# Kernel tuning notes

Hardware: AMD Instinct MI355X
Metric: run time of the kernel (lower is better)

## Reference

```python
import jax, jax.numpy as jnp
import numpy as np

N_EMBD = 768
N_HEAD = 12
HEAD_DIM = N_EMBD // N_HEAD


def setup_inputs() -> dict:
    key = jax.random.key(0)
    k1, k2, k3, k4, k5 = jax.random.split(key, 5)
    B, T, C = 8, 1024, N_EMBD
    s = 0.02
    return {
        "x": jax.random.normal(k1, (B, T, C), dtype=jnp.float32),
        "w_attn": jax.random.normal(k2, (C, 3 * C), dtype=jnp.float32) * s,
        "b_attn": jnp.zeros((3 * C,), dtype=jnp.float32),
        "w_proj": jax.random.normal(k3, (C, C), dtype=jnp.float32) * s,
        "b_proj": jnp.zeros((C,), dtype=jnp.float32),
    }


def reference(x, w_attn, b_attn, w_proj, b_proj):
    B, T, C = x.shape
    H, D = N_HEAD, HEAD_DIM
    qkv = x @ w_attn + b_attn                      # [B,T,3C]
    q, k, v = jnp.split(qkv, 3, axis=-1)
    # [B,H,T,D]
    q = q.reshape(B, T, H, D).transpose(0, 2, 1, 3)
    k = k.reshape(B, T, H, D).transpose(0, 2, 1, 3)
    v = v.reshape(B, T, H, D).transpose(0, 2, 1, 3)
    att = jnp.einsum("bhqd,bhkd->bhqk", q, k) / jnp.sqrt(jnp.float32(D))
    causal = jnp.tril(jnp.ones((T, T), dtype=bool))
    att = jnp.where(causal[None, None], att, jnp.float32(-jnp.inf))
    att = jax.nn.softmax(att, axis=-1)
    y = jnp.einsum("bhqk,bhkd->bhqd", att, v)      # [B,H,T,D]
    y = y.transpose(0, 2, 1, 3).reshape(B, T, C)
    return y @ w_proj + b_proj
```

## Files before the change

kernel.cpp:

```cpp
#include <hip/hip_runtime.h>
#include <hip/hip_bf16.h>
#include <math.h>
#include <type_traits>

#define BATCH 8
#define SEQ   1024
#define NEMBD 768
#define NHEAD 12
#define HDIM  64
#define TC    (3 * NEMBD)

typedef __attribute__((ext_vector_type(4))) float f32x4;
typedef __attribute__((ext_vector_type(8))) short s16x8;

__device__ __forceinline__ unsigned short f2bf(float f) {
    return __builtin_bit_cast(unsigned short, __float2bfloat16(f));
}

__device__ __forceinline__ void gload_lds16(const void* g, void* l) {
    __builtin_amdgcn_global_load_lds(
        (const __attribute__((address_space(1))) void*)g,
        (__attribute__((address_space(3))) void*)l, 16, 0, 0);
}

__global__ __launch_bounds__(256) void cast_bf16_kernel(
    const float* __restrict__ in, unsigned short* __restrict__ out, int n)
{
    const int i = (blockIdx.x * 256 + threadIdx.x) * 8;
    float4 a = *(const float4*)(in + i);
    float4 b = *(const float4*)(in + i + 4);
    s16x8 v;
    v[0] = f2bf(a.x); v[1] = f2bf(a.y); v[2] = f2bf(a.z); v[3] = f2bf(a.w);
    v[4] = f2bf(b.x); v[5] = f2bf(b.y); v[6] = f2bf(b.z); v[7] = f2bf(b.w);
    *(s16x8*)(out + i) = v;
}

__global__ __launch_bounds__(256) void transpose_cast_kernel(
    const float* __restrict__ w, unsigned short* __restrict__ wT, int K, int N)
{
    __shared__ float t[32][33];
    const int tx = threadIdx.x, ty = threadIdx.y;
    const int n0 = blockIdx.x * 32, k0 = blockIdx.y * 32;
    #pragma unroll
    for (int i = 0; i < 4; ++i)
        t[ty + i * 8][tx] = w[(size_t)(k0 + ty + i * 8) * N + n0 + tx];
    __syncthreads();
    #pragma unroll
    for (int i = 0; i < 4; ++i)
        wT[(size_t)(n0 + ty + i * 8) * K + k0 + tx] = f2bf(t[tx][ty + i * 8]);
}

template <int OUTK>
__global__ __launch_bounds__(256) void gemm_bk64_kernel(
    const unsigned short* __restrict__ A,
    const unsigned short* __restrict__ Bt,
    const float* __restrict__ bias,
    float* __restrict__ C,
    unsigned short* __restrict__ Qb,
    unsigned short* __restrict__ Kb,
    unsigned short* __restrict__ Vtb,
    int M, int N, int K, int nbn)
{
    __shared__ __align__(16) unsigned short As[128 * 64];
    __shared__ __align__(16) unsigned short Bs[128 * 64];

    const int tid  = threadIdx.x;
    const int w    = tid >> 6, lane = tid & 63;
    const int lr   = lane & 15, lg = lane >> 4;
    const int wr   = w >> 1, wc = w & 1;

    const int swz = (blockIdx.x & 7) * (gridDim.x >> 3) + (blockIdx.x >> 3);
    const int bm = (swz / nbn) * 128, bn = (swz % nbn) * 128;

    const int srow = tid >> 3;
    const int gcol = ((tid & 7) ^ (srow & 7)) * 8;
    const unsigned short* Ag = A  + (size_t)(bm + srow) * K + gcol;
    const unsigned short* Bg = Bt + (size_t)(bn + srow) * K + gcol;
    unsigned short* Al = As + tid * 8;
    unsigned short* Bl = Bs + tid * 8;

    f32x4 acc[4][4];
    #pragma unroll
    for (int m = 0; m < 4; ++m)
        #pragma unroll
        for (int n = 0; n < 4; ++n) acc[m][n] = (f32x4){0.f, 0.f, 0.f, 0.f};

    for (int k0 = 0; k0 < K; k0 += 64) {
        __syncthreads();
        #pragma unroll
        for (int p = 0; p < 4; ++p) {
            gload_lds16(Ag + (size_t)(p * 32) * K + k0, Al + p * 2048);
            gload_lds16(Bg + (size_t)(p * 32) * K + k0, Bl + p * 2048);
        }
        __syncthreads();

        #pragma unroll
        for (int kk = 0; kk < 2; ++kk) {
            s16x8 af[4], bf[4];
            #pragma unroll
            for (int m = 0; m < 4; ++m) {
                const int ar = wr * 64 + m * 16 + lr;
                af[m] = *(const s16x8*)&As[ar * 64 + (((kk * 4 + lg) ^ (ar & 7)) * 8)];
            }
            #pragma unroll
            for (int n = 0; n < 4; ++n) {
                const int br = wc * 64 + n * 16 + lr;
                bf[n] = *(const s16x8*)&Bs[br * 64 + (((kk * 4 + lg) ^ (br & 7)) * 8)];
            }
            __builtin_amdgcn_s_setprio(1);
            #pragma unroll
            for (int m = 0; m < 4; ++m)
                #pragma unroll
                for (int n = 0; n < 4; ++n)
                    acc[m][n] = __builtin_amdgcn_mfma_f32_16x16x32_bf16(
                        af[m], bf[n], acc[m][n], 0, 0, 0);
            __builtin_amdgcn_s_setprio(0);
        }
    }

    if constexpr (OUTK == 0) {
        #pragma unroll
        for (int n = 0; n < 4; ++n) {
            const int col = bn + wc * 64 + n * 16 + lr;
            const float bv = bias[col];
            #pragma unroll
            for (int m = 0; m < 4; ++m) {
                const int row0 = bm + wr * 64 + m * 16 + lg * 4;
                #pragma unroll
                for (int r = 0; r < 4; ++r)
                    C[(size_t)(row0 + r) * N + col] = acc[m][n][r] + bv;
            }
        }
    } else {
        __syncthreads();
        char* Ep = (char*)((w < 2 ? As : Bs)) + (w & 1) * 8192;

        const int region = bn / NEMBD;
        const int hh = ((bn % NEMBD) >> 6) + wc;
        const int row0 = bm + wr * 64;
        const int bb = row0 >> 10, t0 = row0 & 1023;

        float bvn[4];
        #pragma unroll
        for (int n = 0; n < 4; ++n) bvn[n] = bias[bn + wc * 64 + n * 16 + lr];

        if (region == 2) {
            #pragma unroll
            for (int m = 0; m < 4; ++m)
                #pragma unroll
                for (int n = 0; n < 4; ++n) {
                    ushort4 pk;
                    pk.x = f2bf(acc[m][n][0] + bvn[n]);
                    pk.y = f2bf(acc[m][n][1] + bvn[n]);
                    pk.z = f2bf(acc[m][n][2] + bvn[n]);
                    pk.w = f2bf(acc[m][n][3] + bvn[n]);
                    const int row = n * 16 + lr;
                    const int lc  = m * 2 + (lg >> 1);
                    *(ushort4*)(Ep + row * 128 + ((lc ^ (lr & 7)) * 16)
                                   + (lg & 1) * 8) = pk;
                }
        } else {
            #pragma unroll
            for (int m = 0; m < 4; ++m)
                #pragma unroll
                for (int n = 0; n < 4; ++n)
                    #pragma unroll
                    for (int r = 0; r < 4; ++r) {
                        const int row = m * 16 + lg * 4 + r;
                        const int lc  = n * 2 + (lr >> 3);
                        *(unsigned short*)(Ep + row * 128
                            + ((lc ^ (row & 7)) * 16) + (lr & 7) * 2) =
                            f2bf(acc[m][n][r] + bvn[n]);
                    }
        }
        asm volatile("s_waitcnt lgkmcnt(0)" ::: "memory");
        __builtin_amdgcn_sched_barrier(0);

        const int rr0 = lane >> 3;
        const int cc  = lane & 7;
        if (region == 2) {
            unsigned short* dst = Vtb + (((size_t)bb * NHEAD + hh) * HDIM) * SEQ + t0;
            #pragma unroll
            for (int it = 0; it < 8; ++it) {
                const int d = it * 8 + rr0;
                s16x8 v = *(const s16x8*)(Ep + d * 128 + ((cc ^ (d & 7)) * 16));
                *(s16x8*)(dst + (size_t)d * SEQ + cc * 8) = v;
            }
        } else {
            unsigned short* dst = (region == 0 ? Qb : Kb)
                                + ((size_t)bb * NHEAD + hh) * SEQ * HDIM;
            #pragma unroll
            for (int it = 0; it < 8; ++it) {
                const int t = it * 8 + rr0;
                s16x8 v = *(const s16x8*)(Ep + t * 128 + ((cc ^ (t & 7)) * 16));
                *(s16x8*)(dst + (size_t)(t0 + t) * HDIM + cc * 8) = v;
            }
        }
    }
}

__global__ __launch_bounds__(256) void attn_mfma_kernel(
    const unsigned short* __restrict__ Qb,
    const unsigned short* __restrict__ Kb,
    const unsigned short* __restrict__ Vtb,
    unsigned short* __restrict__ y)
{
    const int bid = blockIdx.x;
    const int xcd = bid & 7;
    const int grp = bid >> 3;
    const int qt  = 15 - (grp & 15);
    const int bh  = xcd + 8 * (grp >> 4);
    const int b   = bh / NHEAD, h = bh % NHEAD;

    const int tid  = threadIdx.x;
    const int w    = tid >> 6;
    const int lane = tid & 63;
    const int lr   = lane & 15;
    const int lg   = lane >> 4;

    __shared__ __align__(16) unsigned short Ks[64 * 64];
    __shared__ __align__(16) unsigned short Vs[64 * 64];
    __shared__ __align__(16) unsigned short Ps[4][16][72];

    const unsigned short* Qg = Qb  + ((size_t)bh * SEQ + qt * 64 + w * 16) * HDIM;
    const unsigned short* Kg = Kb  + (size_t)bh * SEQ * HDIM;
    const unsigned short* Vg = Vtb + (size_t)bh * HDIM * SEQ;

    s16x8 qf[2];
    #pragma unroll
    for (int kc = 0; kc < 2; ++kc)
        qf[kc] = *(const s16x8*)(Qg + (size_t)lr * HDIM + kc * 32 + lg * 8);

    f32x4 acc[4];
    #pragma unroll
    for (int df = 0; df < 4; ++df) acc[df] = (f32x4){0.f, 0.f, 0.f, 0.f};
    float mrow = -INFINITY, lrow = 0.f;

    const int sr = tid >> 2;
    const int sc = (tid & 3) * 16;
    const unsigned short* Kgr = Kg + (size_t)sr * HDIM + sc;
    const unsigned short* Vgr = Vg + (size_t)sr * SEQ  + sc;
    const int swz0 = sr * 128 + ((sc * 2)      ^ ((sr & 7) << 4));
    const int swz1 = sr * 128 + ((sc * 2 + 16) ^ ((sr & 7) << 4));
    const int xorv = (lr & 7) << 4;

    const int NT   = qt + 1;
    const int qrow = qt * 64 + w * 16 + lr;

    s16x8 krA = *(const s16x8*)(Kgr);
    s16x8 krB = *(const s16x8*)(Kgr + 8);
    s16x8 vrA = *(const s16x8*)(Vgr);
    s16x8 vrB = *(const s16x8*)(Vgr + 8);

    for (int kt = 0; kt < NT; ++kt) {
        __syncthreads();
        *(s16x8*)((char*)Ks + swz0) = krA;
        *(s16x8*)((char*)Ks + swz1) = krB;
        *(s16x8*)((char*)Vs + swz0) = vrA;
        *(s16x8*)((char*)Vs + swz1) = vrB;
        __syncthreads();
        if (kt + 1 < NT) {
            krA = *(const s16x8*)(Kgr + (size_t)(kt + 1) * 64 * HDIM);
            krB = *(const s16x8*)(Kgr + (size_t)(kt + 1) * 64 * HDIM + 8);
            vrA = *(const s16x8*)(Vgr + (kt + 1) * 64);
            vrB = *(const s16x8*)(Vgr + (kt + 1) * 64 + 8);
        }

        f32x4 sf[4];
        __builtin_amdgcn_s_setprio(1);
        #pragma unroll
        for (int s = 0; s < 4; ++s) {
            const int rb = (s * 16 + lr) * 128;
            s16x8 a0 = *(const s16x8*)((const char*)Ks + rb + ((lg * 16) ^ xorv));
            s16x8 a1 = *(const s16x8*)((const char*)Ks + rb + ((64 + lg * 16) ^ xorv));
            sf[s] = __builtin_amdgcn_mfma_f32_16x16x32_bf16(
                a0, qf[0], (f32x4){0.f, 0.f, 0.f, 0.f}, 0, 0, 0);
            sf[s] = __builtin_amdgcn_mfma_f32_16x16x32_bf16(a1, qf[1], sf[s], 0, 0, 0);
        }
        __builtin_amdgcn_s_setprio(0);

        float sv[4][4];
        #pragma unroll
        for (int s = 0; s < 4; ++s)
            #pragma unroll
            for (int r = 0; r < 4; ++r)
                sv[s][r] = sf[s][r] * 0.125f;
        if (kt == NT - 1) {
            const int kbase = kt * 64;
            #pragma unroll
            for (int s = 0; s < 4; ++s)
                #pragma unroll
                for (int r = 0; r < 4; ++r)
                    if (kbase + s * 16 + lg * 4 + r > qrow)
                        sv[s][r] = -INFINITY;
        }

        float mx4[4];
        #pragma unroll
        for (int s = 0; s < 4; ++s)
            mx4[s] = fmaxf(fmaxf(sv[s][0], sv[s][1]), fmaxf(sv[s][2], sv[s][3]));
        float mx = fmaxf(fmaxf(mx4[0], mx4[1]), fmaxf(mx4[2], mx4[3]));
        mx = fmaxf(mx, __shfl_xor(mx, 16, 64));
        mx = fmaxf(mx, __shfl_xor(mx, 32, 64));
        const float mnew = fmaxf(mrow, mx);
        const float al   = __expf(mrow - mnew);
        mrow = mnew;

        float rsum = 0.f;
        #pragma unroll
        for (int s = 0; s < 4; ++s) {
            float p0 = __expf(sv[s][0] - mnew);
            float p1 = __expf(sv[s][1] - mnew);
            float p2 = __expf(sv[s][2] - mnew);
            float p3 = __expf(sv[s][3] - mnew);
            rsum += (p0 + p1) + (p2 + p3);
            ushort4 pk;
            pk.x = f2bf(p0); pk.y = f2bf(p1); pk.z = f2bf(p2); pk.w = f2bf(p3);
            *(ushort4*)&Ps[w][lr][s * 16 + lg * 4] = pk;
        }
        rsum += __shfl_xor(rsum, 16, 64);
        rsum += __shfl_xor(rsum, 32, 64);
        lrow = lrow * al + rsum;

        #pragma unroll
        for (int df = 0; df < 4; ++df) acc[df] *= al;

        asm volatile("s_waitcnt lgkmcnt(0)" ::: "memory");
        __builtin_amdgcn_sched_barrier(0);
        s16x8 pa[2];
        #pragma unroll
        for (int kc = 0; kc < 2; ++kc)
            pa[kc] = *(const s16x8*)&Ps[w][lr][kc * 32 + lg * 8];

        __builtin_amdgcn_s_setprio(1);
        #pragma unroll
        for (int df = 0; df < 4; ++df) {
            const int rb = (df * 16 + lr) * 128;
            s16x8 va0 = *(const s16x8*)((const char*)Vs + rb + ((lg * 16) ^ xorv));
            s16x8 va1 = *(const s16x8*)((const char*)Vs + rb + ((64 + lg * 16) ^ xorv));
            acc[df] = __builtin_amdgcn_mfma_f32_16x16x32_bf16(va0, pa[0], acc[df], 0, 0, 0);
            acc[df] = __builtin_amdgcn_mfma_f32_16x16x32_bf16(va1, pa[1], acc[df], 0, 0, 0);
        }
        __builtin_amdgcn_s_setprio(0);
    }

    const float inv = 1.f / lrow;
    const int t = qt * 64 + w * 16 + lr;
    unsigned short* yp = y + ((size_t)(b * SEQ) + t) * NEMBD + h * HDIM;
    #pragma unroll
    for (int df = 0; df < 4; ++df) {
        ushort4 pk;
        pk.x = f2bf(acc[df][0] * inv);
        pk.y = f2bf(acc[df][1] * inv);
        pk.z = f2bf(acc[df][2] * inv);
        pk.w = f2bf(acc[df][3] * inv);
        *(ushort4*)(yp + df * 16 + lg * 4) = pk;
    }
}

extern "C" void kernel_launch(void* const* d_in, const int* in_sizes, int n_in,
                              void* d_out, int out_size, void* d_ws, size_t ws_size,
                              hipStream_t stream)
{
    const float* x      = (const float*)d_in[0];
    const float* w_attn = (const float*)d_in[1];
    const float* b_attn = (const float*)d_in[2];
    const float* w_proj = (const float*)d_in[3];
    const float* b_proj = (const float*)d_in[4];
    float* out = (float*)d_out;

    const int M = BATCH * SEQ;
    const size_t NQKV = (size_t)M * NEMBD;

    unsigned short* xb  = (unsigned short*)d_ws;
    unsigned short* waT = xb  + NQKV;
    unsigned short* wpT = waT + (size_t)TC * NEMBD;
    unsigned short* Qb  = wpT + (size_t)NEMBD * NEMBD;
    unsigned short* Kb  = Qb  + NQKV;
    unsigned short* Vtb = Kb  + NQKV;
    unsigned short* yb  = Vtb + NQKV;

    cast_bf16_kernel<<<(M * NEMBD) / 2048, 256, 0, stream>>>(x, xb, M * NEMBD);
    transpose_cast_kernel<<<dim3(TC / 32, NEMBD / 32), dim3(32, 8), 0, stream>>>(
        w_attn, waT, NEMBD, TC);
    transpose_cast_kernel<<<dim3(NEMBD / 32, NEMBD / 32), dim3(32, 8), 0, stream>>>(
        w_proj, wpT, NEMBD, NEMBD);

    gemm_bk64_kernel<1><<<(TC / 128) * (M / 128), 256, 0, stream>>>(
        xb, waT, b_attn, nullptr, Qb, Kb, Vtb, M, TC, NEMBD, TC / 128);

    attn_mfma_kernel<<<16 * NHEAD * BATCH, 256, 0, stream>>>(Qb, Kb, Vtb, yb);

    gemm_bk64_kernel<0><<<(NEMBD / 128) * (M / 128), 256, 0, stream>>>(
        yb, wpT, b_proj, out, nullptr, nullptr, nullptr, M, NEMBD, NEMBD, NEMBD / 128);
}
```

Measured before the change: 117.3 us.

## Triple-buffer GEMM LDS loads with BK=32 and one barrier per step

Replaces the single-buffered BK=64 GEMM main loop with a 3-stage BK=32 software pipeline. Global-to-LDS async loads for tile t+2 are issued before the MFMAs on tile t, with vmcnt waits and one barrier per iteration instead of two syncthreads. The LDS swizzle is adapted to 64-byte rows. The goal is to hide global memory latency behind MFMA work. The cost is more LDS (48KB) and smaller K steps, which can lower occupancy and add per-iteration overhead.

```diff
diff --git a/kernel.cpp b/kernel.cpp
--- a/kernel.cpp
+++ b/kernel.cpp
@@ -51,7 +51,7 @@
 }
 
 template <int OUTK>
-__global__ __launch_bounds__(256) void gemm_bk64_kernel(
+__global__ __launch_bounds__(256) void gemm_pipe3_kernel(
     const unsigned short* __restrict__ A,
     const unsigned short* __restrict__ Bt,
     const float* __restrict__ bias,
@@ -61,8 +61,8 @@
     unsigned short* __restrict__ Vtb,
     int M, int N, int K, int nbn)
 {
-    __shared__ __align__(16) unsigned short As[128 * 64];
-    __shared__ __align__(16) unsigned short Bs[128 * 64];
+    constexpr int BUF = 16384;
+    __shared__ __align__(16) char SM[3 * BUF];
 
     const int tid  = threadIdx.x;
     const int w    = tid >> 6, lane = tid & 63;
@@ -72,12 +72,12 @@
     const int swz = (blockIdx.x & 7) * (gridDim.x >> 3) + (blockIdx.x >> 3);
     const int bm = (swz / nbn) * 128, bn = (swz % nbn) * 128;
 
-    const int srow = tid >> 3;
-    const int gcol = ((tid & 7) ^ (srow & 7)) * 8;
+    const int srow = tid >> 2;
+    const int gcol = ((tid & 3) ^ ((srow >> 1) & 3)) * 8;
     const unsigned short* Ag = A  + (size_t)(bm + srow) * K + gcol;
     const unsigned short* Bg = Bt + (size_t)(bn + srow) * K + gcol;
-    unsigned short* Al = As + tid * 8;
-    unsigned short* Bl = Bs + tid * 8;
+
+    const int NT = K >> 5;
 
     f32x4 acc[4][4];
     #pragma unroll
@@ -85,37 +85,58 @@
         #pragma unroll
         for (int n = 0; n < 4; ++n) acc[m][n] = (f32x4){0.f, 0.f, 0.f, 0.f};
 
-    for (int k0 = 0; k0 < K; k0 += 64) {
-        __syncthreads();
-        #pragma unroll
-        for (int p = 0; p < 4; ++p) {
-            gload_lds16(Ag + (size_t)(p * 32) * K + k0, Al + p * 2048);
-            gload_lds16(Bg + (size_t)(p * 32) * K + k0, Bl + p * 2048);
-        }
-        __syncthreads();
-
-        #pragma unroll
-        for (int kk = 0; kk < 2; ++kk) {
-            s16x8 af[4], bf[4];
-            #pragma unroll
-            for (int m = 0; m < 4; ++m) {
-                const int ar = wr * 64 + m * 16 + lr;
-                af[m] = *(const s16x8*)&As[ar * 64 + (((kk * 4 + lg) ^ (ar & 7)) * 8)];
-            }
-            #pragma unroll
-            for (int n = 0; n < 4; ++n) {
-                const int br = wc * 64 + n * 16 + lr;
-                bf[n] = *(const s16x8*)&Bs[br * 64 + (((kk * 4 + lg) ^ (br & 7)) * 8)];
-            }
-            __builtin_amdgcn_s_setprio(1);
-            #pragma unroll
-            for (int m = 0; m < 4; ++m)
-                #pragma unroll
-                for (int n = 0; n < 4; ++n)
-                    acc[m][n] = __builtin_amdgcn_mfma_f32_16x16x32_bf16(
-                        af[m], bf[n], acc[m][n], 0, 0, 0);
-            __builtin_amdgcn_s_setprio(0);
-        }
+    auto stage = [&](int t) {
+        const int k0 = t << 5;
+        char* buf = SM + (t % 3) * BUF;
+        #pragma unroll
+        for (int p = 0; p < 2; ++p)
+            gload_lds16(Ag + (size_t)(p * 64) * K + k0,
+                        buf + p * 4096 + tid * 16);
+        #pragma unroll
+        for (int p = 0; p < 2; ++p)
+            gload_lds16(Bg + (size_t)(p * 64) * K + k0,
+                        buf + 8192 + p * 4096 + tid * 16);
+    };
+
+    stage(0);
+    stage(1);
+    asm volatile("s_waitcnt vmcnt(4)" ::: "memory");
+    __builtin_amdgcn_sched_barrier(0);
+    __builtin_amdgcn_s_barrier();
+    __builtin_amdgcn_sched_barrier(0);
+
+    for (int t = 0; t < NT; ++t) {
+        const char* buf = SM + (t % 3) * BUF;
+        const bool more = (t + 2 < NT);
+        if (more) stage(t + 2);
+
+        s16x8 af[4], bfr[4];
+        #pragma unroll
+        for (int m = 0; m < 4; ++m) {
+            const int ar = wr * 64 + m * 16 + lr;
+            af[m] = *(const s16x8*)(buf + ar * 64 + ((lg ^ ((ar >> 1) & 3)) * 16));
+        }
+        #pragma unroll
+        for (int n = 0; n < 4; ++n) {
+            const int br = wc * 64 + n * 16 + lr;
+            bfr[n] = *(const s16x8*)(buf + 8192 + br * 64
+                                         + ((lg ^ ((br >> 1) & 3)) * 16));
+        }
+
+        __builtin_amdgcn_s_setprio(1);
+        #pragma unroll
+        for (int m = 0; m < 4; ++m)
+            #pragma unroll
+            for (int n = 0; n < 4; ++n)
+                acc[m][n] = __builtin_amdgcn_mfma_f32_16x16x32_bf16(
+                    af[m], bfr[n], acc[m][n], 0, 0, 0);
+        __builtin_amdgcn_s_setprio(0);
+
+        if (more) asm volatile("s_waitcnt vmcnt(4)" ::: "memory");
+        else      asm volatile("s_waitcnt vmcnt(0)" ::: "memory");
+        __builtin_amdgcn_sched_barrier(0);
+        __builtin_amdgcn_s_barrier();
+        __builtin_amdgcn_sched_barrier(0);
     }
 
     if constexpr (OUTK == 0) {
@@ -132,8 +153,7 @@
             }
         }
     } else {
-        __syncthreads();
-        char* Ep = (char*)((w < 2 ? As : Bs)) + (w & 1) * 8192;
+        char* Ep = SM + w * 8192;
 
         const int region = bn / NEMBD;
         const int hh = ((bn % NEMBD) >> 6) + wc;
@@ -386,11 +406,11 @@
     transpose_cast_kernel<<<dim3(NEMBD / 32, NEMBD / 32), dim3(32, 8), 0, stream>>>(
         w_proj, wpT, NEMBD, NEMBD);
 
-    gemm_bk64_kernel<1><<<(TC / 128) * (M / 128), 256, 0, stream>>>(
+    gemm_pipe3_kernel<1><<<(TC / 128) * (M / 128), 256, 0, stream>>>(
         xb, waT, b_attn, nullptr, Qb, Kb, Vtb, M, TC, NEMBD, TC / 128);
 
     attn_mfma_kernel<<<16 * NHEAD * BATCH, 256, 0, stream>>>(Qb, Kb, Vtb, yb);
 
-    gemm_bk64_kernel<0><<<(NEMBD / 128) * (M / 128), 256, 0, stream>>>(
+    gemm_pipe3_kernel<0><<<(NEMBD / 128) * (M / 128), 256, 0, stream>>>(
         yb, wpT, b_proj, out, nullptr, nullptr, nullptr, M, NEMBD, NEMBD, NEMBD / 128);
 }
```

Result: no change. 116.9 us (-0.4%).
